# Kernel optimization log

Hardware: AMD Instinct MI355X
Metric: run time of the kernel (lower is better)

## Reference

```python
import jax, jax.numpy as jnp
import numpy as np

BS, D, M = 64, 256, 512


def setup_inputs() -> dict:
    key = jax.random.key(0)
    ks = jax.random.split(key, 6)
    # Small scales keep the 10-step RLS recurrence numerically stable.
    A_start = 0.05 * jax.random.normal(ks[0], (BS, D, D), dtype=jnp.float32)
    Y1 = 0.05 * jax.random.normal(ks[1], (BS, D, M), dtype=jnp.float32)
    Y2 = 0.05 * jax.random.normal(ks[2], (BS, D, M), dtype=jnp.float32)
    y1 = 0.05 * jax.random.normal(ks[3], (BS, D, 1), dtype=jnp.float32)
    y2 = 0.05 * jax.random.normal(ks[4], (BS, D, 1), dtype=jnp.float32)
    eye = jnp.broadcast_to(jnp.eye(D, dtype=jnp.float32), (BS, D, D))
    P_inv_start = 1e-3 * eye + 1e-4 * jax.random.normal(ks[5], (BS, D, D), dtype=jnp.float32)
    return {"A_start": A_start, "Y1": Y1, "Y2": Y2, "y1": y1, "y2": y2,
            "P_inv_start": P_inv_start, "h": 2, "m_prox": 10}


def _t(x):
    return jnp.swapaxes(x, 1, 2)


def reference(A_start, Y1, Y2, y1, y2, P_inv_start, h, m_prox):
    """Faithful jax version of DelayedDMD.update.

    The torch code recomputes `A_t + P_inv @ (Y1 @ (Y2^T - Y1^T @ A_t))` twice
    per step; here it is computed once (same math, fused).
    """
    Y1t, Y2t, y1t, y2t = _t(Y1), _t(Y2), _t(y1), _t(y2)
    denom = 1.0 + y1t @ P_inv_start @ y1          # (bs, 1, 1)
    Piy1 = P_inv_start @ y1                       # (bs, d, 1)

    def step(A_t, _):
        # batch recursive-least-squares prox iteration
        M_ = A_t + P_inv_start @ (Y1 @ (Y2t - Y1t @ A_t))   # (bs, d, d)
        A_new = M_ + y1 @ (y2t - y1t @ M_) / denom
        return A_new, None

    A_final_t, _ = jax.lax.scan(step, _t(A_start), None, length=m_prox)
    P_inv_new = P_inv_start - Piy1 @ (y1t @ P_inv_start) / denom
    return _t(A_final_t), P_inv_new
```

## Files before the change

kernel.cpp:

```cpp
#include <hip/hip_runtime.h>
#include <hip/hip_bf16.h>
#include <stdint.h>


#define BSZ 64
#define DD 256
#define MM 512

typedef __attribute__((ext_vector_type(8))) short short8;
typedef __attribute__((ext_vector_type(4))) float f32x4;

__device__ __forceinline__ unsigned short f2b(float f) {
    unsigned int u = __float_as_uint(f);
    unsigned int r = (u + 0x7fffu + ((u >> 16) & 1u)) >> 16;
    return (unsigned short)r;
}
__device__ __forceinline__ float b2f(unsigned short s) {
    return __uint_as_float(((unsigned int)s) << 16);
}


__global__ __launch_bounds__(256)
void prep1(const float* __restrict__ P, const float* __restrict__ y1g,
           unsigned short* __restrict__ Pb, float* __restrict__ vec,
           float* __restrict__ qpart)
{
    const int blk = blockIdx.x, t = threadIdx.x;
    const int b = blk >> 3, rs = (blk & 7) * 32;
    const long base = (long)b * DD * DD;
    const int wv = t >> 6, ln = t & 63;
    __shared__ float sy1[DD];
    __shared__ float qsh[4][DD];
    sy1[t] = y1g[b * DD + t];
    __syncthreads();
    const int col4 = ln * 4;
    const float4 yv = *(const float4*)(sy1 + col4);
    float4 pr[8];
#pragma unroll
    for (int i = 0; i < 8; ++i) {
        const int row = rs + i * 4 + wv;
        pr[i] = *(const float4*)(P + base + (long)row * DD + col4);
    }
    float ql0 = 0.f, ql1 = 0.f, ql2 = 0.f, ql3 = 0.f;
#pragma unroll
    for (int i = 0; i < 8; ++i) {
        const int row = rs + i * 4 + wv;
        const long o = base + (long)row * DD + col4;
        const float4 p = pr[i];
        ushort4 u;
        u.x = f2b(p.x); u.y = f2b(p.y); u.z = f2b(p.z); u.w = f2b(p.w);
        *(ushort4*)(Pb + o) = u;
        const float yr = sy1[row];
        ql0 += yr * p.x; ql1 += yr * p.y; ql2 += yr * p.z; ql3 += yr * p.w;
        float s = p.x * yv.x + p.y * yv.y + p.z * yv.z + p.w * yv.w;
#pragma unroll
        for (int off = 32; off; off >>= 1) s += __shfl_down(s, off, 64);
        if (ln == 0) vec[(long)b * 768 + row] = s;
    }
    *(float4*)(qsh[wv] + col4) = make_float4(ql0, ql1, ql2, ql3);
    __syncthreads();
    qpart[((long)blk) * DD + t] = qsh[0][t] + qsh[1][t] + qsh[2][t] + qsh[3][t];
}

__global__ __launch_bounds__(256)
void prep2(const float* __restrict__ Y1, const float* __restrict__ Y2,
           const float* __restrict__ y1g, const float* __restrict__ qpart,
           unsigned short* __restrict__ G1b, unsigned short* __restrict__ G21b,
           float* __restrict__ vec)
{
    __shared__ __align__(16) unsigned short As[128 * 64];
    __shared__ __align__(16) unsigned short Bs[128 * 64];
    const int blk = blockIdx.x, t = threadIdx.x;
    if (blk < 512) {
        const int quad = blk & 3, z = blk >> 2, sel = z >> 6, b = z & 63;
        const int i0 = (quad >> 1) * 128, j0 = (quad & 1) * 128;
        const float* Af = (sel ? Y2 : Y1) + (long)b * DD * MM;
        const float* Bf = Y1 + (long)b * DD * MM;
        unsigned short* Ob = (sel ? G21b : G1b) + (long)b * DD * DD;
        const int wv = t >> 6, ln = t & 63;
        const int lr = ln & 15, qd = ln >> 4;
        const int mh = (wv >> 1) * 64, nh = (wv & 1) * 64;
        const int srow = t >> 4, sc4 = t & 15;
        f32x4 acc[4][4] = {};
        float4 fa[8], fb[8];

#define PRE2_ISSUE(kc)                                                          \
        _Pragma("unroll")                                                       \
        for (int i = 0; i < 8; ++i) {                                           \
            const int row = i * 16 + srow;                                      \
            fa[i] = *(const float4*)(Af + (long)(i0 + row) * MM + (kc) * 64 + sc4 * 4); \
            fb[i] = *(const float4*)(Bf + (long)(j0 + row) * MM + (kc) * 64 + sc4 * 4); \
        }

        PRE2_ISSUE(0);
        for (int kc = 0; kc < 8; ++kc) {
#pragma unroll
            for (int i = 0; i < 8; ++i) {
                const int row = i * 16 + srow;
                const int cb = (sc4 * 8) ^ ((row & 7) << 4);
                ushort4 ua, ub;
                ua.x = f2b(fa[i].x); ua.y = f2b(fa[i].y); ua.z = f2b(fa[i].z); ua.w = f2b(fa[i].w);
                ub.x = f2b(fb[i].x); ub.y = f2b(fb[i].y); ub.z = f2b(fb[i].z); ub.w = f2b(fb[i].w);
                *(ushort4*)((char*)As + row * 128 + cb) = ua;
                *(ushort4*)((char*)Bs + row * 128 + cb) = ub;
            }
            __syncthreads();
            if (kc < 7) PRE2_ISSUE(kc + 1);
#pragma unroll
            for (int kc2 = 0; kc2 < 2; ++kc2) {
                short8 af[4], bfr[4];
#pragma unroll
                for (int mt = 0; mt < 4; ++mt) {
                    const int row = mh + mt * 16 + lr;
                    af[mt] = *(const short8*)((char*)As + row * 128 +
                                              ((kc2 * 64 + qd * 16) ^ ((row & 7) << 4)));
                }
#pragma unroll
                for (int nt = 0; nt < 4; ++nt) {
                    const int row = nh + nt * 16 + lr;
                    bfr[nt] = *(const short8*)((char*)Bs + row * 128 +
                                               ((kc2 * 64 + qd * 16) ^ ((row & 7) << 4)));
                }
#pragma unroll
                for (int mt = 0; mt < 4; ++mt)
#pragma unroll
                    for (int nt = 0; nt < 4; ++nt)
                        acc[mt][nt] = __builtin_amdgcn_mfma_f32_16x16x32_bf16(
                            af[mt], bfr[nt], acc[mt][nt], 0, 0, 0);
            }
            __syncthreads();
        }
#undef PRE2_ISSUE
#pragma unroll
        for (int mt = 0; mt < 4; ++mt)
#pragma unroll
            for (int nt = 0; nt < 4; ++nt) {
                const int gr0 = i0 + mh + mt * 16 + qd * 4;
                const int gc  = j0 + nh + nt * 16 + lr;
#pragma unroll
                for (int r = 0; r < 4; ++r)
                    Ob[(long)(gr0 + r) * DD + gc] = f2b(acc[mt][nt][r]);
            }
        return;
    }
    const int b = blk - 512;
    float* vb = vec + (long)b * 768;
    const float* qp = qpart + (long)b * 8 * DD;
    float qv = 0.f;
#pragma unroll
    for (int c = 0; c < 8; ++c) qv += qp[c * DD + t];
    vb[256 + t] = qv;
    __shared__ float red[256];
    red[t] = vb[t] * y1g[b * DD + t];
    __syncthreads();
    for (int s = 128; s; s >>= 1) { if (t < s) red[t] += red[t + s]; __syncthreads(); }
    if (t == 0) vb[512] = 1.0f / (1.0f + red[0]);
}

__global__ __launch_bounds__(256)
void gemmEV(const unsigned short* __restrict__ Pb, const unsigned short* __restrict__ G1b,
            const unsigned short* __restrict__ G21b,
            const float* __restrict__ y1g, const float* __restrict__ y2g,
            const float* __restrict__ vec,
            unsigned short* __restrict__ Enb, unsigned short* __restrict__ Vpb)
{
    __shared__ __align__(16) unsigned short As[128 * 128];
    __shared__ __align__(16) unsigned short Bs[128 * 128];
    __shared__ float qs[DD], s1[DD], s2[DD];
    const int blk = blockIdx.x, t = threadIdx.x;
    const int quad = blk & 3, z = blk >> 2, sel = z >> 6, b = z & 63;
    const int i0 = (quad >> 1) * 128, j0 = (quad & 1) * 128;
    const unsigned short* Ab = (sel ? G21b : Pb) + (long)b * DD * DD;
    const unsigned short* Bb = (sel ? Pb : G1b) + (long)b * DD * DD;
    unsigned short* Ob = (sel ? Vpb : Enb) + (long)b * DD * DD;
    const float* vb = vec + (long)b * 768;
    const int wv = t >> 6, ln = t & 63;
    const int lr = ln & 15, qd = ln >> 4;
    const int mh = (wv >> 1) * 64, nh = (wv & 1) * 64;
    const int srow = t >> 4, sc16 = t & 15;

    qs[t] = vb[256 + t];
    s1[t] = y1g[b * DD + t];
    s2[t] = y2g[b * DD + t];

    f32x4 acc[4][4] = {};
    float dot[4] = {0.f, 0.f, 0.f, 0.f};
    uint4 ra[8], rb[8];

#define GEV_ISSUE(kc)                                                           \
    _Pragma("unroll")                                                           \
    for (int i = 0; i < 8; ++i) {                                               \
        const int row = i * 16 + srow;                                          \
        ra[i] = *(const uint4*)(Ab + (long)(i0 + row) * DD + (kc) * 128 + sc16 * 8); \
        rb[i] = *(const uint4*)(Bb + (long)(j0 + row) * DD + (kc) * 128 + sc16 * 8); \
    }

    GEV_ISSUE(0);
#pragma unroll
    for (int kc = 0; kc < 2; ++kc) {
#pragma unroll
        for (int i = 0; i < 8; ++i) {
            const int row = i * 16 + srow;
            const int cb = (sc16 * 16) ^ ((row & 7) << 4);
            *(uint4*)((char*)As + row * 256 + cb) = ra[i];
            *(uint4*)((char*)Bs + row * 256 + cb) = rb[i];
        }
        __syncthreads();
        if (kc == 0) GEV_ISSUE(1);
#pragma unroll
        for (int kc2 = 0; kc2 < 4; ++kc2) {
            short8 af[4], bfr[4];
#pragma unroll
            for (int mt = 0; mt < 4; ++mt) {
                const int row = mh + mt * 16 + lr;
                af[mt] = *(const short8*)((char*)As + row * 256 +
                                          ((kc2 * 64 + qd * 16) ^ ((row & 7) << 4)));
            }
#pragma unroll
            for (int nt = 0; nt < 4; ++nt) {
                const int row = nh + nt * 16 + lr;
                bfr[nt] = *(const short8*)((char*)Bs + row * 256 +
                                           ((kc2 * 64 + qd * 16) ^ ((row & 7) << 4)));
            }
            const int kb = kc * 128 + kc2 * 32;
            const float4 qa = *(const float4*)(qs + kb + qd * 8);
            const float4 qb = *(const float4*)(qs + kb + qd * 8 + 4);
            const float qf[8] = {qa.x, qa.y, qa.z, qa.w, qb.x, qb.y, qb.z, qb.w};
            if (!sel) {
#pragma unroll
                for (int nt = 0; nt < 4; ++nt)
#pragma unroll
                    for (int j = 0; j < 8; ++j)
                        dot[nt] += b2f((unsigned short)bfr[nt][j]) * qf[j];
            } else {
#pragma unroll
                for (int mt = 0; mt < 4; ++mt)
#pragma unroll
                    for (int j = 0; j < 8; ++j)
                        dot[mt] += b2f((unsigned short)af[mt][j]) * qf[j];
            }
#pragma unroll
            for (int mt = 0; mt < 4; ++mt)
#pragma unroll
                for (int nt = 0; nt < 4; ++nt)
                    acc[mt][nt] = __builtin_amdgcn_mfma_f32_16x16x32_bf16(
                        af[mt], bfr[nt], acc[mt][nt], 0, 0, 0);
        }
        __syncthreads();
    }
#undef GEV_ISSUE
#pragma unroll
    for (int i = 0; i < 4; ++i) {
        dot[i] += __shfl_xor(dot[i], 16, 64);
        dot[i] += __shfl_xor(dot[i], 32, 64);
    }
    const float kk = vb[512];
#pragma unroll
    for (int mt = 0; mt < 4; ++mt) {
#pragma unroll
        for (int nt = 0; nt < 4; ++nt) {
            const int gr0 = i0 + mh + mt * 16 + qd * 4;
            const int gc  = j0 + nh + nt * 16 + lr;
            if (!sel) {
                const float cw = s1[gc] - dot[nt];
#pragma unroll
                for (int r = 0; r < 4; ++r) {
                    const float rv = kk * s1[gr0 + r];
                    Ob[(long)(gr0 + r) * DD + gc] = f2b(-(acc[mt][nt][r] + rv * cw));
                }
            } else {
                const float cv = s1[gc];
#pragma unroll
                for (int r = 0; r < 4; ++r) {
                    const float uv = __shfl(dot[mt], qd * 4 + r, 64);
                    const float rv = kk * (s2[gr0 + r] - uv);
                    Ob[(long)(gr0 + r) * DD + gc] = f2b(acc[mt][nt][r] + rv * cv);
                }
            }
        }
    }
}

#define SWZ(row) (((row) ^ ((row) >> 3)) & 7)
__global__ __launch_bounds__(256, 2)
void iterk(const float* __restrict__ A_start, const unsigned short* __restrict__ Enb,
           const unsigned short* __restrict__ Vpb,
           const float* __restrict__ P, const float* __restrict__ vec,
           float* __restrict__ out1, float* __restrict__ out2)
{
    const int blk = blockIdx.x, t = threadIdx.x;
    if (blk >= 512) {
        const int c = blk - 512, b = c >> 2, rs = (c & 3) * 64;
        const long base = (long)b * DD * DD;
        const float* vb = vec + (long)b * 768;
        const float kk = vb[512];
#pragma unroll 4
        for (int i = 0; i < 16; ++i) {
            const int idx = rs * DD + (i * 256 + t) * 4;
            const int row = idx >> 8, col = idx & 255;
            const float kPi = kk * vb[row];
            float4 p = *(const float4*)(P + base + idx);
            float4 q = *(const float4*)(vb + 256 + col);
            float4 rr;
            rr.x = p.x - kPi * q.x; rr.y = p.y - kPi * q.y;
            rr.z = p.z - kPi * q.z; rr.w = p.w - kPi * q.w;
            *(float4*)(out2 + base + idx) = rr;
        }
        return;
    }
    __shared__ __align__(16) unsigned short Ash[32 * 256];
    const int b = blk >> 3, r0 = (blk & 7) * 32;
    const long base = (long)b * DD * DD;
    const float* Ab = A_start + base;
    const unsigned short* Eb = Enb + base;
    const unsigned short* Vb = Vpb + base;
    float* Ob = out1 + base;
    const int wv = t >> 6, ln = t & 63;
    const int lr = ln & 15, qd = ln >> 4;

    f32x4 acc[2][4], vv[2][4];
    short8 ef[4][8];

#pragma unroll
    for (int mt = 0; mt < 2; ++mt)
#pragma unroll
        for (int j = 0; j < 4; ++j) {
            const int col = wv * 64 + j * 16 + lr;
            const int rowb = r0 + mt * 16 + qd * 4;
#pragma unroll
            for (int r = 0; r < 4; ++r) {
                const long o = (long)(rowb + r) * DD + col;
                acc[mt][j][r] = Ab[o];
                vv[mt][j][r]  = b2f(Vb[o]);
            }
        }
#pragma unroll
    for (int j = 0; j < 4; ++j) {
        const int n = wv * 64 + j * 16 + lr;
#pragma unroll
        for (int kc = 0; kc < 8; ++kc)
            ef[j][kc] = *(const short8*)(Eb + (long)n * DD + kc * 32 + qd * 8);
    }

#pragma unroll 1
    for (int s = 0; s < 10; ++s) {
        const int cgb = wv * 8 + (lr >> 3), cb = lr & 7;
#pragma unroll
        for (int mt = 0; mt < 2; ++mt)
#pragma unroll
            for (int j = 0; j < 4; ++j) {
#pragma unroll
                for (int r = 0; r < 4; ++r) {
                    const int lrow = mt * 16 + qd * 4 + r;
                    const int cg = (cgb + j * 2) ^ SWZ(lrow);
                    Ash[lrow * 256 + cg * 8 + cb] = f2b(acc[mt][j][r]);
                }
                acc[mt][j] += vv[mt][j];
            }
        __syncthreads();
#pragma unroll
        for (int kc = 0; kc < 8; ++kc) {
            short8 af[2];
#pragma unroll
            for (int mt = 0; mt < 2; ++mt) {
                const int row = mt * 16 + lr;
                const int cg = (kc * 4 + qd) ^ SWZ(row);
                af[mt] = *(const short8*)(Ash + row * 256 + cg * 8);
            }
#pragma unroll
            for (int mt = 0; mt < 2; ++mt)
#pragma unroll
                for (int j = 0; j < 4; ++j)
                    acc[mt][j] = __builtin_amdgcn_mfma_f32_16x16x32_bf16(
                        af[mt], ef[j][kc], acc[mt][j], 0, 0, 0);
        }
        __syncthreads();
    }

#pragma unroll
    for (int mt = 0; mt < 2; ++mt)
#pragma unroll
        for (int j = 0; j < 4; ++j) {
            const int col = wv * 64 + j * 16 + lr;
            const int rowb = r0 + mt * 16 + qd * 4;
#pragma unroll
            for (int r = 0; r < 4; ++r)
                Ob[(long)(rowb + r) * DD + col] = acc[mt][j][r];
        }
}

extern "C" void kernel_launch(void* const* d_in, const int* in_sizes, int n_in,
                              void* d_out, int out_size, void* d_ws, size_t ws_size,
                              hipStream_t stream)
{
    const float* A_start = (const float*)d_in[0];
    const float* Y1      = (const float*)d_in[1];
    const float* Y2      = (const float*)d_in[2];
    const float* y1      = (const float*)d_in[3];
    const float* y2      = (const float*)d_in[4];
    const float* P       = (const float*)d_in[5];

    const long EL2 = (long)BSZ * DD * DD;

    float* out1 = (float*)d_out;
    float* out2 = out1 + EL2;

    char* w8 = (char*)d_ws;
    unsigned short* Pb    = (unsigned short*)(w8);
    unsigned short* G1b   = (unsigned short*)(w8 + 8388608);
    unsigned short* G21b  = (unsigned short*)(w8 + 16777216);
    unsigned short* Enb   = (unsigned short*)(w8 + 25165824);
    unsigned short* Vpb   = (unsigned short*)(w8 + 33554432);
    float*          vec   = (float*)(w8 + 41943040);
    float*          qpart = (float*)(w8 + 42139648);

    const dim3 blk(256);

    prep1<<<512, blk, 0, stream>>>(P, y1, Pb, vec, qpart);
    prep2<<<576, blk, 0, stream>>>(Y1, Y2, y1, qpart, G1b, G21b, vec);
    gemmEV<<<512, blk, 0, stream>>>(Pb, G1b, G21b, y1, y2, vec, Enb, Vpb);
    iterk<<<768, blk, 0, stream>>>(A_start, Enb, Vpb, P, vec, out1, out2);
}
```

Measured before the change: 225.4 us.

## Pre-convert Y1/Y2 to bf16, fuse G1/G21 GEMMs, use direct global-to-LDS loads

A new pass in the first kernel converts Y1 and Y2 to bf16 in workspace. The Gram GEMM kernel then computes Y1·Y1ᵀ and Y2·Y1ᵀ in the same block, sharing the Y1 B-tile, and loads its operands with global_load_lds into double-buffered LDS. gemmEV gets the same double-buffered direct-to-LDS load path. Block indices are remapped in gemmEV and iterk so that blocks from the same batch are interleaved in launch order, likely for cache locality. The cost is an extra bf16 round trip of Y1 and Y2 through memory and higher register and LDS use in the fused GEMM.

```diff
diff --git a/kernel.cpp b/kernel.cpp
--- a/kernel.cpp
+++ b/kernel.cpp
@@ -18,14 +18,36 @@
 __device__ __forceinline__ float b2f(unsigned short s) {
     return __uint_as_float(((unsigned int)s) << 16);
 }
+__device__ __forceinline__ void gll16(const void* g, void* l) {
+    __builtin_amdgcn_global_load_lds(
+        (const __attribute__((address_space(1))) unsigned int*)g,
+        (__attribute__((address_space(3))) unsigned int*)l, 16, 0, 0);
+}
 
 
 __global__ __launch_bounds__(256)
-void prep1(const float* __restrict__ P, const float* __restrict__ y1g,
-           unsigned short* __restrict__ Pb, float* __restrict__ vec,
-           float* __restrict__ qpart)
+void prep1c(const float* __restrict__ P, const float* __restrict__ y1g,
+            const float* __restrict__ Y1, const float* __restrict__ Y2,
+            unsigned short* __restrict__ Pb, unsigned short* __restrict__ Y1b,
+            unsigned short* __restrict__ Y2b,
+            float* __restrict__ vec, float* __restrict__ qpart)
 {
     const int blk = blockIdx.x, t = threadIdx.x;
+    if (blk >= 512) {
+        const int c = blk - 512;
+        const float* src = (c < 512) ? Y1 : Y2;
+        unsigned short* dst = (c < 512) ? Y1b : Y2b;
+        const long base = (long)(c & 511) * 16384;
+#pragma unroll 4
+        for (int i = 0; i < 16; ++i) {
+            const long idx = base + (long)(i * 256 + t) * 4;
+            const float4 v = *(const float4*)(src + idx);
+            ushort4 u;
+            u.x = f2b(v.x); u.y = f2b(v.y); u.z = f2b(v.z); u.w = f2b(v.w);
+            *(ushort4*)(dst + idx) = u;
+        }
+        return;
+    }
     const int b = blk >> 3, rs = (blk & 7) * 32;
     const long base = (long)b * DD * DD;
     const int wv = t >> 6, ln = t & 63;
@@ -63,98 +85,99 @@
 }
 
 __global__ __launch_bounds__(256)
-void prep2(const float* __restrict__ Y1, const float* __restrict__ Y2,
+void prep2(const unsigned short* __restrict__ Y1b, const unsigned short* __restrict__ Y2b,
            const float* __restrict__ y1g, const float* __restrict__ qpart,
            unsigned short* __restrict__ G1b, unsigned short* __restrict__ G21b,
            float* __restrict__ vec)
 {
-    __shared__ __align__(16) unsigned short As[128 * 64];
-    __shared__ __align__(16) unsigned short Bs[128 * 64];
     const int blk = blockIdx.x, t = threadIdx.x;
-    if (blk < 512) {
-        const int quad = blk & 3, z = blk >> 2, sel = z >> 6, b = z & 63;
-        const int i0 = (quad >> 1) * 128, j0 = (quad & 1) * 128;
-        const float* Af = (sel ? Y2 : Y1) + (long)b * DD * MM;
-        const float* Bf = Y1 + (long)b * DD * MM;
-        unsigned short* Ob = (sel ? G21b : G1b) + (long)b * DD * DD;
-        const int wv = t >> 6, ln = t & 63;
-        const int lr = ln & 15, qd = ln >> 4;
-        const int mh = (wv >> 1) * 64, nh = (wv & 1) * 64;
-        const int srow = t >> 4, sc4 = t & 15;
-        f32x4 acc[4][4] = {};
-        float4 fa[8], fb[8];
-
-#define PRE2_ISSUE(kc)                                                          \
-        _Pragma("unroll")                                                       \
-        for (int i = 0; i < 8; ++i) {                                           \
-            const int row = i * 16 + srow;                                      \
-            fa[i] = *(const float4*)(Af + (long)(i0 + row) * MM + (kc) * 64 + sc4 * 4); \
-            fb[i] = *(const float4*)(Bf + (long)(j0 + row) * MM + (kc) * 64 + sc4 * 4); \
-        }
-
-        PRE2_ISSUE(0);
-        for (int kc = 0; kc < 8; ++kc) {
-#pragma unroll
-            for (int i = 0; i < 8; ++i) {
-                const int row = i * 16 + srow;
-                const int cb = (sc4 * 8) ^ ((row & 7) << 4);
-                ushort4 ua, ub;
-                ua.x = f2b(fa[i].x); ua.y = f2b(fa[i].y); ua.z = f2b(fa[i].z); ua.w = f2b(fa[i].w);
-                ub.x = f2b(fb[i].x); ub.y = f2b(fb[i].y); ub.z = f2b(fb[i].z); ub.w = f2b(fb[i].w);
-                *(ushort4*)((char*)As + row * 128 + cb) = ua;
-                *(ushort4*)((char*)Bs + row * 128 + cb) = ub;
-            }
-            __syncthreads();
-            if (kc < 7) PRE2_ISSUE(kc + 1);
-#pragma unroll
-            for (int kc2 = 0; kc2 < 2; ++kc2) {
-                short8 af[4], bfr[4];
-#pragma unroll
-                for (int mt = 0; mt < 4; ++mt) {
-                    const int row = mh + mt * 16 + lr;
-                    af[mt] = *(const short8*)((char*)As + row * 128 +
-                                              ((kc2 * 64 + qd * 16) ^ ((row & 7) << 4)));
+    if (blk >= 256) {
+        const int b = blk - 256;
+        float* vb = vec + (long)b * 768;
+        const float* qp = qpart + (long)b * 8 * DD;
+        float qv = 0.f;
+#pragma unroll
+        for (int c = 0; c < 8; ++c) qv += qp[c * DD + t];
+        vb[256 + t] = qv;
+        __shared__ float red[256];
+        red[t] = vb[t] * y1g[b * DD + t];
+        __syncthreads();
+        for (int s = 128; s; s >>= 1) { if (t < s) red[t] += red[t + s]; __syncthreads(); }
+        if (t == 0) vb[512] = 1.0f / (1.0f + red[0]);
+        return;
+    }
+    __shared__ __align__(16) unsigned short S[2][3][128 * 64];
+    const int b = (blk & 7) + 8 * (blk >> 5), quad = (blk >> 3) & 3;
+    const int i0 = (quad >> 1) * 128, j0 = (quad & 1) * 128;
+    const char* A1 = (const char*)(Y1b + (long)b * DD * MM + (long)i0 * MM);
+    const char* A2 = (const char*)(Y2b + (long)b * DD * MM + (long)i0 * MM);
+    const char* By = (const char*)(Y1b + (long)b * DD * MM + (long)j0 * MM);
+    const int wv = t >> 6, ln = t & 63;
+    const int lr = ln & 15, qd = ln >> 4;
+    const int mh = (wv >> 1) * 64, nh = (wv & 1) * 64;
+    const int srow = t >> 3;
+    const int sc = (t & 7) * 16;
+    f32x4 acc1[4][4] = {}, acc2[4][4] = {};
+
+#define P2STAGE(u, kc)                                                            \
+    _Pragma("unroll")                                                             \
+    for (int i = 0; i < 4; ++i) {                                                 \
+        const int row = i * 32 + srow;                                            \
+        const int gco = (kc) * 128 + (sc ^ ((row & 7) << 4));                     \
+        const int lo = row * 128 + sc;                                            \
+        gll16(A1 + (long)row * 1024 + gco, (char*)S[u][0] + lo);                  \
+        gll16(A2 + (long)row * 1024 + gco, (char*)S[u][1] + lo);                  \
+        gll16(By + (long)row * 1024 + gco, (char*)S[u][2] + lo);                  \
+    }
+
+    P2STAGE(0, 0);
+    for (int kc = 0; kc < 8; ++kc) {
+        __syncthreads();
+        if (kc < 7) { P2STAGE((kc + 1) & 1, kc + 1); }
+        const unsigned short (*Su)[128 * 64] = S[kc & 1];
+#pragma unroll
+        for (int kc2 = 0; kc2 < 2; ++kc2) {
+            const int kb = kc2 * 64 + qd * 16;
+            short8 a1[4], a2[4], bf[4];
+#pragma unroll
+            for (int mt = 0; mt < 4; ++mt) {
+                const int row = mh + mt * 16 + lr;
+                const int o = row * 128 + (kb ^ ((row & 7) << 4));
+                a1[mt] = *(const short8*)((const char*)Su[0] + o);
+                a2[mt] = *(const short8*)((const char*)Su[1] + o);
+            }
+#pragma unroll
+            for (int nt = 0; nt < 4; ++nt) {
+                const int row = nh + nt * 16 + lr;
+                bf[nt] = *(const short8*)((const char*)Su[2] + row * 128 +
+                                          (kb ^ ((row & 7) << 4)));
+            }
+#pragma unroll
+            for (int mt = 0; mt < 4; ++mt)
+#pragma unroll
+                for (int nt = 0; nt < 4; ++nt) {
+                    acc1[mt][nt] = __builtin_amdgcn_mfma_f32_16x16x32_bf16(
+                        a1[mt], bf[nt], acc1[mt][nt], 0, 0, 0);
+                    acc2[mt][nt] = __builtin_amdgcn_mfma_f32_16x16x32_bf16(
+                        a2[mt], bf[nt], acc2[mt][nt], 0, 0, 0);
                 }
-#pragma unroll
-                for (int nt = 0; nt < 4; ++nt) {
-                    const int row = nh + nt * 16 + lr;
-                    bfr[nt] = *(const short8*)((char*)Bs + row * 128 +
-                                               ((kc2 * 64 + qd * 16) ^ ((row & 7) << 4)));
-                }
-#pragma unroll
-                for (int mt = 0; mt < 4; ++mt)
-#pragma unroll
-                    for (int nt = 0; nt < 4; ++nt)
-                        acc[mt][nt] = __builtin_amdgcn_mfma_f32_16x16x32_bf16(
-                            af[mt], bfr[nt], acc[mt][nt], 0, 0, 0);
-            }
-            __syncthreads();
-        }
-#undef PRE2_ISSUE
-#pragma unroll
-        for (int mt = 0; mt < 4; ++mt)
-#pragma unroll
-            for (int nt = 0; nt < 4; ++nt) {
-                const int gr0 = i0 + mh + mt * 16 + qd * 4;
-                const int gc  = j0 + nh + nt * 16 + lr;
-#pragma unroll
-                for (int r = 0; r < 4; ++r)
-                    Ob[(long)(gr0 + r) * DD + gc] = f2b(acc[mt][nt][r]);
-            }
-        return;
-    }
-    const int b = blk - 512;
-    float* vb = vec + (long)b * 768;
-    const float* qp = qpart + (long)b * 8 * DD;
-    float qv = 0.f;
-#pragma unroll
-    for (int c = 0; c < 8; ++c) qv += qp[c * DD + t];
-    vb[256 + t] = qv;
-    __shared__ float red[256];
-    red[t] = vb[t] * y1g[b * DD + t];
-    __syncthreads();
-    for (int s = 128; s; s >>= 1) { if (t < s) red[t] += red[t + s]; __syncthreads(); }
-    if (t == 0) vb[512] = 1.0f / (1.0f + red[0]);
+        }
+    }
+#undef P2STAGE
+    unsigned short* O1 = G1b  + (long)b * DD * DD;
+    unsigned short* O2 = G21b + (long)b * DD * DD;
+#pragma unroll
+    for (int mt = 0; mt < 4; ++mt)
+#pragma unroll
+        for (int nt = 0; nt < 4; ++nt) {
+            const int gr0 = i0 + mh + mt * 16 + qd * 4;
+            const int gc  = j0 + nh + nt * 16 + lr;
+#pragma unroll
+            for (int r = 0; r < 4; ++r) {
+                O1[(long)(gr0 + r) * DD + gc] = f2b(acc1[mt][nt][r]);
+                O2[(long)(gr0 + r) * DD + gc] = f2b(acc2[mt][nt][r]);
+            }
+        }
 }
 
 __global__ __launch_bounds__(256)
@@ -164,20 +187,21 @@
             const float* __restrict__ vec,
             unsigned short* __restrict__ Enb, unsigned short* __restrict__ Vpb)
 {
-    __shared__ __align__(16) unsigned short As[128 * 128];
-    __shared__ __align__(16) unsigned short Bs[128 * 128];
+    __shared__ __align__(16) unsigned short S[2][2][128 * 64];
     __shared__ float qs[DD], s1[DD], s2[DD];
     const int blk = blockIdx.x, t = threadIdx.x;
-    const int quad = blk & 3, z = blk >> 2, sel = z >> 6, b = z & 63;
+    const int b = (blk & 7) + 8 * (blk >> 6);
+    const int rem = (blk >> 3) & 7, sel = rem >> 2, quad = rem & 3;
     const int i0 = (quad >> 1) * 128, j0 = (quad & 1) * 128;
-    const unsigned short* Ab = (sel ? G21b : Pb) + (long)b * DD * DD;
-    const unsigned short* Bb = (sel ? Pb : G1b) + (long)b * DD * DD;
+    const char* Ab = (const char*)((sel ? G21b : Pb) + (long)b * DD * DD + (long)i0 * DD);
+    const char* Bb = (const char*)((sel ? Pb : G1b) + (long)b * DD * DD + (long)j0 * DD);
     unsigned short* Ob = (sel ? Vpb : Enb) + (long)b * DD * DD;
     const float* vb = vec + (long)b * 768;
     const int wv = t >> 6, ln = t & 63;
     const int lr = ln & 15, qd = ln >> 4;
     const int mh = (wv >> 1) * 64, nh = (wv & 1) * 64;
-    const int srow = t >> 4, sc16 = t & 15;
+    const int srow = t >> 3;
+    const int sc = (t & 7) * 16;
 
     qs[t] = vb[256 + t];
     s1[t] = y1g[b * DD + t];
@@ -185,46 +209,41 @@
 
     f32x4 acc[4][4] = {};
     float dot[4] = {0.f, 0.f, 0.f, 0.f};
-    uint4 ra[8], rb[8];
-
-#define GEV_ISSUE(kc)                                                           \
-    _Pragma("unroll")                                                           \
-    for (int i = 0; i < 8; ++i) {                                               \
-        const int row = i * 16 + srow;                                          \
-        ra[i] = *(const uint4*)(Ab + (long)(i0 + row) * DD + (kc) * 128 + sc16 * 8); \
-        rb[i] = *(const uint4*)(Bb + (long)(j0 + row) * DD + (kc) * 128 + sc16 * 8); \
-    }
-
-    GEV_ISSUE(0);
-#pragma unroll
-    for (int kc = 0; kc < 2; ++kc) {
-#pragma unroll
-        for (int i = 0; i < 8; ++i) {
-            const int row = i * 16 + srow;
-            const int cb = (sc16 * 16) ^ ((row & 7) << 4);
-            *(uint4*)((char*)As + row * 256 + cb) = ra[i];
-            *(uint4*)((char*)Bs + row * 256 + cb) = rb[i];
-        }
+
+#define GEVSTAGE(u, kc)                                                           \
+    _Pragma("unroll")                                                             \
+    for (int i = 0; i < 4; ++i) {                                                 \
+        const int row = i * 32 + srow;                                            \
+        const int gco = (kc) * 128 + (sc ^ ((row & 7) << 4));                     \
+        const int lo = row * 128 + sc;                                            \
+        gll16(Ab + (long)row * 512 + gco, (char*)S[u][0] + lo);                   \
+        gll16(Bb + (long)row * 512 + gco, (char*)S[u][1] + lo);                   \
+    }
+
+    GEVSTAGE(0, 0);
+    for (int kc = 0; kc < 4; ++kc) {
         __syncthreads();
-        if (kc == 0) GEV_ISSUE(1);
-#pragma unroll
-        for (int kc2 = 0; kc2 < 4; ++kc2) {
+        if (kc < 3) { GEVSTAGE((kc + 1) & 1, kc + 1); }
+        const unsigned short (*Su)[128 * 64] = S[kc & 1];
+#pragma unroll
+        for (int kc2 = 0; kc2 < 2; ++kc2) {
+            const int kb = kc2 * 64 + qd * 16;
             short8 af[4], bfr[4];
 #pragma unroll
             for (int mt = 0; mt < 4; ++mt) {
                 const int row = mh + mt * 16 + lr;
-                af[mt] = *(const short8*)((char*)As + row * 256 +
-                                          ((kc2 * 64 + qd * 16) ^ ((row & 7) << 4)));
+                af[mt] = *(const short8*)((const char*)Su[0] + row * 128 +
+                                          (kb ^ ((row & 7) << 4)));
             }
 #pragma unroll
             for (int nt = 0; nt < 4; ++nt) {
                 const int row = nh + nt * 16 + lr;
-                bfr[nt] = *(const short8*)((char*)Bs + row * 256 +
-                                           ((kc2 * 64 + qd * 16) ^ ((row & 7) << 4)));
-            }
-            const int kb = kc * 128 + kc2 * 32;
-            const float4 qa = *(const float4*)(qs + kb + qd * 8);
-            const float4 qb = *(const float4*)(qs + kb + qd * 8 + 4);
+                bfr[nt] = *(const short8*)((const char*)Su[1] + row * 128 +
+                                           (kb ^ ((row & 7) << 4)));
+            }
+            const int kel = kc * 64 + kc2 * 32 + qd * 8;
+            const float4 qa = *(const float4*)(qs + kel);
+            const float4 qb = *(const float4*)(qs + kel + 4);
             const float qf[8] = {qa.x, qa.y, qa.z, qa.w, qb.x, qb.y, qb.z, qb.w};
             if (!sel) {
 #pragma unroll
@@ -246,9 +265,8 @@
                     acc[mt][nt] = __builtin_amdgcn_mfma_f32_16x16x32_bf16(
                         af[mt], bfr[nt], acc[mt][nt], 0, 0, 0);
         }
-        __syncthreads();
-    }
-#undef GEV_ISSUE
+    }
+#undef GEVSTAGE
 #pragma unroll
     for (int i = 0; i < 4; ++i) {
         dot[i] += __shfl_xor(dot[i], 16, 64);
@@ -309,7 +327,7 @@
         return;
     }
     __shared__ __align__(16) unsigned short Ash[32 * 256];
-    const int b = blk >> 3, r0 = (blk & 7) * 32;
+    const int b = (blk & 7) + 8 * (blk >> 6), r0 = ((blk >> 3) & 7) * 32;
     const long base = (long)b * DD * DD;
     const float* Ab = A_start + base;
     const unsigned short* Eb = Enb + base;
@@ -411,13 +429,15 @@
     unsigned short* G21b  = (unsigned short*)(w8 + 16777216);
     unsigned short* Enb   = (unsigned short*)(w8 + 25165824);
     unsigned short* Vpb   = (unsigned short*)(w8 + 33554432);
-    float*          vec   = (float*)(w8 + 41943040);
-    float*          qpart = (float*)(w8 + 42139648);
+    unsigned short* Y1b   = (unsigned short*)(w8 + 41943040);
+    unsigned short* Y2b   = (unsigned short*)(w8 + 58720256);
+    float*          vec   = (float*)(w8 + 75497472);
+    float*          qpart = (float*)(w8 + 75694080);
 
     const dim3 blk(256);
 
-    prep1<<<512, blk, 0, stream>>>(P, y1, Pb, vec, qpart);
-    prep2<<<576, blk, 0, stream>>>(Y1, Y2, y1, qpart, G1b, G21b, vec);
+    prep1c<<<1536, blk, 0, stream>>>(P, y1, Y1, Y2, Pb, Y1b, Y2b, vec, qpart);
+    prep2<<<320, blk, 0, stream>>>(Y1b, Y2b, y1, qpart, G1b, G21b, vec);
     gemmEV<<<512, blk, 0, stream>>>(Pb, G1b, G21b, y1, y2, vec, Enb, Vpb);
     iterk<<<768, blk, 0, stream>>>(A_start, Enb, Vpb, P, vec, out1, out2);
 }
```

Result: faster. 213.5 us (-5.3%).
